# Kernel tuning notes

Hardware: AMD Instinct MI355X
Metric: run time of the kernel (lower is better)

The kernel has to match this reference:

```python
import jax, jax.numpy as jnp
import numpy as np

# UKF constants (Merwe scaled sigma points)
ALPHA, BETA, KAPPA = 1.0, 2.0, 0.0
JITTER = 1e-4
S_DIM, C_DIM, M_DIM, H_DIM = 8, 2, 4, 32


def setup_inputs() -> dict:
    B, T = 1024, 256
    key = jax.random.key(0)
    ks = jax.random.split(key, 11)
    inp = {
        "X0": 0.1 * jax.random.normal(ks[0], (B, S_DIM), dtype=jnp.float32),
        "u": jax.random.normal(ks[1], (B, T, C_DIM), dtype=jnp.float32),
        "y": jax.random.normal(ks[2], (B, T, M_DIM), dtype=jnp.float32),
        # learned process model f(x,u) = x + tanh([x;u] W1 + b1) W2 + b2
        "W1": 0.1 * jax.random.normal(ks[3], (S_DIM + C_DIM, H_DIM), dtype=jnp.float32),
        "b1": jnp.zeros((H_DIM,), dtype=jnp.float32),
        "W2": 0.1 * jax.random.normal(ks[4], (H_DIM, S_DIM), dtype=jnp.float32),
        "b2": jnp.zeros((S_DIM,), dtype=jnp.float32),
        # linear measurement model h(x) = Hm x
        "Hm": 0.3 * jax.random.normal(ks[5], (M_DIM, S_DIM), dtype=jnp.float32),
        # learned diagonal noise / initial covariance (softplus parameterized)
        "lq": -3.0 + 0.1 * jax.random.normal(ks[6], (S_DIM,), dtype=jnp.float32),
        "lr": -2.0 + 0.1 * jax.random.normal(ks[7], (M_DIM,), dtype=jnp.float32),
        "lp0": -1.0 + 0.1 * jax.random.normal(ks[8], (S_DIM,), dtype=jnp.float32),
    }
    return inp


def reference(X0, u, y, W1, b1, W2, b2, Hm, lq, lr, lp0):
    B, n = X0.shape
    T = u.shape[1]
    lam = ALPHA ** 2 * (n + KAPPA) - n
    c = n + lam
    Wm = jnp.concatenate([jnp.array([lam / c], dtype=X0.dtype),
                          jnp.full((2 * n,), 0.5 / c, dtype=X0.dtype)])
    Wc = Wm.at[0].add(1.0 - ALPHA ** 2 + BETA)
    I = jnp.eye(n, dtype=X0.dtype)

    Q = jnp.diag(jax.nn.softplus(lq))            # [n,n] process noise
    R = jnp.diag(jax.nn.softplus(lr))            # [m,m] measurement noise
    P0 = jnp.broadcast_to(jnp.diag(jax.nn.softplus(lp0)), (B, n, n))  # P0(X0)

    def f(pts, u_t):  # pts [B,2n+1,n], u_t [B,C]
        uu = jnp.broadcast_to(u_t[:, None, :], pts.shape[:2] + (u_t.shape[-1],))
        z = jnp.concatenate([pts, uu], axis=-1)
        return pts + jnp.tanh(z @ W1 + b1) @ W2 + b2

    def step(carry, inp_t):
        x, P = carry            # x [B,n], P [B,n,n]
        u_t, y_t = inp_t        # u at i-1, y at i
        # sigma points via Cholesky of scaled covariance
        L = jnp.linalg.cholesky(c * P + JITTER * I)
        offs = jnp.swapaxes(L, -1, -2)  # [B,n,n]: row i = i-th column of L
        pts = jnp.concatenate([x[:, None], x[:, None] + offs, x[:, None] - offs], axis=1)  # [B,2n+1,n]
        # predict
        pts_f = f(pts, u_t)
        x_pred = jnp.einsum('s,bsn->bn', Wm, pts_f)
        dx = pts_f - x_pred[:, None]
        P_pred = jnp.einsum('s,bsn,bsm->bnm', Wc, dx, dx) + Q
        P_pred = 0.5 * (P_pred + jnp.swapaxes(P_pred, -1, -2)) + JITTER * I
        # measurement update (linear h reused on propagated sigma points)
        y_pts = pts_f @ Hm.T
        y_pred = jnp.einsum('s,bsm->bm', Wm, y_pts)
        dy = y_pts - y_pred[:, None]
        Sy = jnp.einsum('s,bsi,bsj->bij', Wc, dy, dy) + R
        Sy = 0.5 * (Sy + jnp.swapaxes(Sy, -1, -2))
        Pxy = jnp.einsum('s,bsn,bsm->bnm', Wc, dx, dy)
        # K = Pxy Sy^{-1} via solve on Sy (SPD)
        K = jnp.swapaxes(jnp.linalg.solve(Sy, jnp.swapaxes(Pxy, -1, -2)), -1, -2)
        x_new = x_pred + jnp.einsum('bnm,bm->bn', K, y_t - y_pred)
        P_new = P_pred - K @ Sy @ jnp.swapaxes(K, -1, -2)
        P_new = 0.5 * (P_new + jnp.swapaxes(P_new, -1, -2)) + JITTER * I
        q_e = 0.5 * jnp.linalg.slogdet(P_pred)[1]  # [B]
        r_e = 0.5 * jnp.linalg.slogdet(Sy)[1]      # [B]
        return (x_new, P_new), (x_new, P_new, q_e, r_e)

    # steps i = 1..T-1 use u[:, i-1] and y[:, i]
    u_seq = jnp.swapaxes(u[:, :T - 1], 0, 1)  # [T-1,B,C]
    y_seq = jnp.swapaxes(y[:, 1:], 0, 1)      # [T-1,B,M]
    _, (Xs, Ps, qs, rs) = jax.lax.scan(step, (X0, P0), (u_seq, y_seq))

    X = jnp.concatenate([X0[:, None], jnp.swapaxes(Xs, 0, 1)], axis=1)        # [B,T,n]
    P = jnp.concatenate([P0[:, None], jnp.swapaxes(Ps, 0, 1)], axis=1)        # [B,T,n,n]
    zcol = jnp.zeros((X0.shape[0], 1), dtype=X0.dtype)
    q_entr = jnp.concatenate([zcol, jnp.swapaxes(qs, 0, 1)], axis=1)          # [B,T]
    r_entr = jnp.concatenate([zcol, jnp.swapaxes(rs, 0, 1)], axis=1)          # [B,T]
    return X, P, q_entr, r_entr
```

## Files before the change

kernel.cpp:

```cpp
#include <hip/hip_runtime.h>
#include <math.h>

#define B_LEN 1024
#define T_LEN 256
#define HST 36

__device__ __forceinline__ float fast_rcp(float x) { return __builtin_amdgcn_rcpf(x); }
__device__ __forceinline__ float fast_rsq(float x) { return __builtin_amdgcn_rsqf(x); }
__device__ __forceinline__ float fast_tanh(float x) {
    float e = __expf(2.0f * x);
    return 1.0f - 2.0f * fast_rcp(e + 1.0f);
}
__device__ __forceinline__ float softplus_f(float x) {
    return (x > 20.0f) ? x : log1pf(expf(x));
}

__global__ __launch_bounds__(128)
void ukf_kernel(const float* __restrict__ X0, const float* __restrict__ U,
                const float* __restrict__ Y,  const float* __restrict__ W1,
                const float* __restrict__ B1, const float* __restrict__ W2,
                const float* __restrict__ B2, const float* __restrict__ HM,
                const float* __restrict__ LQ, const float* __restrict__ LR,
                const float* __restrict__ LP0, float* __restrict__ out)
{
    const int tid  = threadIdx.x;
    const int wid  = tid >> 6;
    const int lane = tid & 63;
    const int b    = blockIdx.x;
    const int i8   = lane >> 3;
    const int j8   = lane & 7;
    const int h32  = lane & 31;
    const int p4   = tid >> 5;
    const int m4   = lane & 3;
    const int sy   = lane >> 2;
    const int s2   = tid >> 3;
    const int d2   = tid & 7;

    __shared__ float u_sh[T_LEN * 2];
    __shared__ float y_sh[T_LEN * 4];
    __shared__ __align__(16) float pts_sh[17 * 8];
    __shared__ __align__(16) float hid_sh[17 * HST];
    __shared__ __align__(16) float pf_sh[17 * 8];
    __shared__ __align__(16) float dx_sh[17 * 8];
    __shared__ __align__(16) float yp_sh[17 * 4];
    __shared__ float x_sh[8];
    __shared__ float xp_sh[8];
    __shared__ float ypred_sh[4];
    __shared__ float Sy_sh[16];
    __shared__ float L4_sh[16];
    __shared__ float Pxy_sh[32];
    __shared__ float K_sh[32];
    __shared__ float T1_sh[32];
    __shared__ float Pp_sh[64];

    for (int k = tid; k < T_LEN * 2; k += 128) u_sh[k] = U[(size_t)b * (T_LEN * 2) + k];
    for (int k = tid; k < T_LEN * 4; k += 128) y_sh[k] = Y[(size_t)b * (T_LEN * 4) + k];

    float w1r[10];
    #pragma unroll
    for (int d = 0; d < 10; ++d) w1r[d] = W1[d * 32 + h32];
    const float b1r = B1[h32];
    float w2r[32];
    #pragma unroll
    for (int h = 0; h < 32; ++h) w2r[h] = W2[h * 8 + d2];
    const float b2r = B2[d2];
    float hmr[8];
    #pragma unroll
    for (int d = 0; d < 8; ++d) hmr[d] = HM[m4 * 8 + d];

    const float qdiag = softplus_f(LQ[i8]);
    const float rdiag = softplus_f(LR[m4]);

    const size_t Xbase = (size_t)b * T_LEN * 8;
    const size_t Pbase = (size_t)B_LEN * T_LEN * 8  + (size_t)b * T_LEN * 64;
    const size_t qbase = (size_t)B_LEN * T_LEN * 72 + (size_t)b * T_LEN;
    const size_t rbase = (size_t)B_LEN * T_LEN * 73 + (size_t)b * T_LEN;

    float P = (i8 == j8) ? softplus_f(LP0[i8]) : 0.0f;
    if (tid < 8) x_sh[tid] = X0[b * 8 + tid];
    if (wid == 0) {
        if (lane < 8) out[Xbase + lane] = X0[b * 8 + lane];
        out[Pbase + lane] = P;
        if (lane == 0) { out[qbase] = 0.0f; out[rbase] = 0.0f; }
    }
    __syncthreads();

    for (int t = 1; t < T_LEN; ++t) {
        if (wid == 0) {
            float a = 8.0f * P + ((i8 == j8) ? 1e-4f : 0.0f);
            #pragma unroll
            for (int j = 0; j < 8; ++j) {
                float dj = __shfl(a, j * 9);
                float rv = fast_rsq(dj);
                if (j8 == j) a = (i8 == j) ? dj * rv : a * rv;
                float ci = __shfl(a, i8 * 8 + j);
                float cj = __shfl(a, j8 * 8 + j);
                if (i8 > j && j8 > j) a -= ci * cj;
            }
            const float Lx = (j8 <= i8) ? a : 0.0f;
            const float xi = x_sh[i8];
            if (j8 == 0) pts_sh[i8] = xi;
            pts_sh[(1 + j8) * 8 + i8] = xi + Lx;
            pts_sh[(9 + j8) * 8 + i8] = xi - Lx;
        }
        __syncthreads();

        {
            const float u0 = u_sh[(t - 1) * 2 + 0];
            const float u1 = u_sh[(t - 1) * 2 + 1];
            const float ub = b1r + u0 * w1r[8] + u1 * w1r[9];
            #pragma unroll
            for (int k = 0; k < 5; ++k) {
                int s = 4 * k + p4;
                if (s < 17) {
                    const float4 pa = *(const float4*)&pts_sh[s * 8];
                    const float4 pb = *(const float4*)&pts_sh[s * 8 + 4];
                    float acc = ub
                        + pa.x * w1r[0] + pa.y * w1r[1] + pa.z * w1r[2] + pa.w * w1r[3]
                        + pb.x * w1r[4] + pb.y * w1r[5] + pb.z * w1r[6] + pb.w * w1r[7];
                    hid_sh[s * HST + h32] = fast_tanh(acc);
                }
            }
        }
        __syncthreads();

        {
            float acc = b2r;
            #pragma unroll
            for (int h = 0; h < 32; h += 4) {
                const float4 hv = *(const float4*)&hid_sh[s2 * HST + h];
                acc += hv.x * w2r[h] + hv.y * w2r[h + 1] + hv.z * w2r[h + 2] + hv.w * w2r[h + 3];
            }
            pf_sh[s2 * 8 + d2] = pts_sh[s2 * 8 + d2] + acc;
            if (tid < 8) {
                float a16 = b2r;
                #pragma unroll
                for (int h = 0; h < 32; h += 4) {
                    const float4 hv = *(const float4*)&hid_sh[16 * HST + h];
                    a16 += hv.x * w2r[h] + hv.y * w2r[h + 1] + hv.z * w2r[h + 2] + hv.w * w2r[h + 3];
                }
                pf_sh[16 * 8 + tid] = pts_sh[16 * 8 + tid] + a16;
            }
        }
        __syncthreads();

        if (wid == 0) {
            const float v0   = pf_sh[i8 * 8 + j8];
            const float v1   = pf_sh[(8 + i8) * 8 + j8];
            const float pf16 = (i8 == 0) ? pf_sh[16 * 8 + j8] : 0.0f;
            float part = ((i8 == 0) ? pf16 : v0) + v1;
            part += __shfl_xor(part, 8);
            part += __shfl_xor(part, 16);
            part += __shfl_xor(part, 32);
            const float xp = part * 0.0625f;
            if (i8 == 0) xp_sh[j8] = xp;
            dx_sh[i8 * 8 + j8]       = v0 - xp;
            dx_sh[(8 + i8) * 8 + j8] = v1 - xp;
            if (i8 == 0) dx_sh[16 * 8 + j8] = pf16 - xp;
        } else {
            float yv0, yv16 = 0.0f;
            {
                const float4 pa = *(const float4*)&pf_sh[sy * 8];
                const float4 pb = *(const float4*)&pf_sh[sy * 8 + 4];
                yv0 = pa.x * hmr[0] + pa.y * hmr[1] + pa.z * hmr[2] + pa.w * hmr[3]
                    + pb.x * hmr[4] + pb.y * hmr[5] + pb.z * hmr[6] + pb.w * hmr[7];
            }
            if (sy == 0) {
                const float4 pa = *(const float4*)&pf_sh[16 * 8];
                const float4 pb = *(const float4*)&pf_sh[16 * 8 + 4];
                yv16 = pa.x * hmr[0] + pa.y * hmr[1] + pa.z * hmr[2] + pa.w * hmr[3]
                     + pb.x * hmr[4] + pb.y * hmr[5] + pb.z * hmr[6] + pb.w * hmr[7];
            }
            float py = (sy == 0) ? yv16 : yv0;
            py += __shfl_xor(py, 4);
            py += __shfl_xor(py, 8);
            py += __shfl_xor(py, 16);
            py += __shfl_xor(py, 32);
            const float ypred = py * 0.0625f;
            if (lane < 4) ypred_sh[lane] = ypred;
            yp_sh[sy * 4 + m4] = yv0 - ypred;
            if (sy == 0) yp_sh[16 * 4 + m4] = yv16 - ypred;
        }
        __syncthreads();

        float Ppred = 0.0f;
        if (wid == 0) {
            float pp = 0.0f;
            #pragma unroll
            for (int s = 1; s < 17; ++s)
                pp += dx_sh[s * 8 + i8] * dx_sh[s * 8 + j8];
            pp *= 0.0625f;
            pp += 2.0f * dx_sh[i8] * dx_sh[j8];
            Ppred = pp + ((i8 == j8) ? (qdiag + 1e-4f) : 0.0f);
            Pp_sh[lane] = Ppred;
        } else {
            if (lane < 16) {
                float acc = 0.0f;
                #pragma unroll
                for (int s = 1; s < 17; ++s)
                    acc += yp_sh[s * 4 + sy] * yp_sh[s * 4 + m4];
                Sy_sh[lane] = acc * 0.0625f + 2.0f * yp_sh[sy] * yp_sh[m4]
                            + ((sy == m4) ? rdiag : 0.0f);
            } else if (lane < 48) {
                const int idx = lane - 16;
                const int ii = idx >> 2, mm = idx & 3;
                float acc = 0.0f;
                #pragma unroll
                for (int s = 1; s < 17; ++s)
                    acc += dx_sh[s * 8 + ii] * yp_sh[s * 4 + mm];
                Pxy_sh[idx] = acc * 0.0625f + 2.0f * dx_sh[ii] * yp_sh[mm];
            }
        }
        __syncthreads();

        if (wid == 0) {
            float l4v = (lane < 16) ? Sy_sh[lane] : 0.0f;
            float re = 0.0f;
            #pragma unroll
            for (int j = 0; j < 4; ++j) {
                float dj = __shfl(l4v, j * 5);
                float rv = fast_rsq(dj);
                re += 0.5f * __logf(dj);
                if (lane < 16 && m4 == j) l4v = (sy == j) ? dj * rv : l4v * rv;
                float ci = __shfl(l4v, (sy * 4 + j) & 63);
                float cj = __shfl(l4v, (m4 * 4 + j) & 63);
                if (lane < 16 && sy > j && m4 > j) l4v -= ci * cj;
            }
            if (lane < 16) L4_sh[lane] = l4v;

            if (lane < 8) {
                const float p0  = Pxy_sh[lane * 4 + 0];
                const float p1  = Pxy_sh[lane * 4 + 1];
                const float p2v = Pxy_sh[lane * 4 + 2];
                const float p3  = Pxy_sh[lane * 4 + 3];
                const float L00 = L4_sh[0],  L10 = L4_sh[4],  L11 = L4_sh[5];
                const float L20 = L4_sh[8],  L21 = L4_sh[9],  L22 = L4_sh[10];
                const float L30 = L4_sh[12], L31 = L4_sh[13], L32 = L4_sh[14], L33 = L4_sh[15];
                const float r0 = fast_rcp(L00), r1 = fast_rcp(L11);
                const float r2 = fast_rcp(L22), r3 = fast_rcp(L33);
                const float w0_ = p0 * r0;
                const float w1_ = (p1 - L10 * w0_) * r1;
                const float w2_ = (p2v - L20 * w0_ - L21 * w1_) * r2;
                const float w3_ = (p3 - L30 * w0_ - L31 * w1_ - L32 * w2_) * r3;
                const float k3 = w3_ * r3;
                const float k2 = (w2_ - L32 * k3) * r2;
                const float k1 = (w1_ - L21 * k2 - L31 * k3) * r1;
                const float k0 = (w0_ - L10 * k1 - L20 * k2 - L30 * k3) * r0;
                K_sh[lane * 4 + 0] = k0;
                K_sh[lane * 4 + 1] = k1;
                K_sh[lane * 4 + 2] = k2;
                K_sh[lane * 4 + 3] = k3;
            }
            if (lane < 32) {
                const int ii = lane >> 2, aa = lane & 3;
                T1_sh[lane] = K_sh[ii * 4 + 0] * Sy_sh[0 + aa]
                            + K_sh[ii * 4 + 1] * Sy_sh[4 + aa]
                            + K_sh[ii * 4 + 2] * Sy_sh[8 + aa]
                            + K_sh[ii * 4 + 3] * Sy_sh[12 + aa];
            }
            float m_ = Ppred - (T1_sh[i8 * 4 + 0] * K_sh[j8 * 4 + 0]
                              + T1_sh[i8 * 4 + 1] * K_sh[j8 * 4 + 1]
                              + T1_sh[i8 * 4 + 2] * K_sh[j8 * 4 + 2]
                              + T1_sh[i8 * 4 + 3] * K_sh[j8 * 4 + 3]);
            float mT = __shfl(m_, j8 * 8 + i8);
            P = 0.5f * (m_ + mT) + ((i8 == j8) ? 1e-4f : 0.0f);
            out[Pbase + (size_t)t * 64 + lane] = P;

            if (lane < 8) {
                const float in0 = y_sh[t * 4 + 0] - ypred_sh[0];
                const float in1 = y_sh[t * 4 + 1] - ypred_sh[1];
                const float in2 = y_sh[t * 4 + 2] - ypred_sh[2];
                const float in3 = y_sh[t * 4 + 3] - ypred_sh[3];
                const float xn = xp_sh[lane]
                    + K_sh[lane * 4 + 0] * in0 + K_sh[lane * 4 + 1] * in1
                    + K_sh[lane * 4 + 2] * in2 + K_sh[lane * 4 + 3] * in3;
                x_sh[lane] = xn;
                out[Xbase + (size_t)t * 8 + lane] = xn;
            }
            if (lane == 0) out[rbase + t] = re;
        } else {
            float ap = Pp_sh[lane];
            float qe = 0.0f;
            #pragma unroll
            for (int j = 0; j < 8; ++j) {
                float dj = __shfl(ap, j * 9);
                float rv = fast_rsq(dj);
                qe += 0.5f * __logf(dj);
                if (j8 == j) ap = (i8 == j) ? dj * rv : ap * rv;
                float ci = __shfl(ap, i8 * 8 + j);
                float cj = __shfl(ap, j8 * 8 + j);
                if (i8 > j && j8 > j) ap -= ci * cj;
            }
            if (lane == 0) out[qbase + t] = qe;
        }
    }
}

extern "C" void kernel_launch(void* const* d_in, const int* in_sizes, int n_in,
                              void* d_out, int out_size, void* d_ws, size_t ws_size,
                              hipStream_t stream) {
    (void)in_sizes; (void)n_in; (void)out_size; (void)d_ws; (void)ws_size;
    const float* X0 = (const float*)d_in[0];
    const float* U  = (const float*)d_in[1];
    const float* Y  = (const float*)d_in[2];
    const float* W1 = (const float*)d_in[3];
    const float* B1 = (const float*)d_in[4];
    const float* W2 = (const float*)d_in[5];
    const float* B2 = (const float*)d_in[6];
    const float* HM = (const float*)d_in[7];
    const float* LQ = (const float*)d_in[8];
    const float* LR = (const float*)d_in[9];
    const float* LP0 = (const float*)d_in[10];
    float* out = (float*)d_out;
    ukf_kernel<<<dim3(B_LEN), dim3(128), 0, stream>>>(X0, U, Y, W1, B1, W2, B2,
                                                      HM, LQ, LR, LP0, out);
}
```

Baseline: 982.1 us.

## Keep covariance columns in registers and use readlane-based Cholesky

Covariance and state now live per-lane as column registers (each lane holds a column across eight rows). The 8x8 and 4x4 Cholesky factorizations use scalar readlane broadcasts instead of shuffles, and the 4x4 factor is computed redundantly in registers instead of going through shared memory. The MLP hidden and output stages are fused into one phase, removing a barrier, and launch bounds now request two blocks per CU. The goal is to cut shuffle and LDS traffic and barriers on the sequential per-timestep critical path, at the cost of more registers and redundant arithmetic across lanes.

```diff
diff --git a/kernel.cpp b/kernel.cpp
--- a/kernel.cpp
+++ b/kernel.cpp
@@ -7,6 +7,9 @@
 
 __device__ __forceinline__ float fast_rcp(float x) { return __builtin_amdgcn_rcpf(x); }
 __device__ __forceinline__ float fast_rsq(float x) { return __builtin_amdgcn_rsqf(x); }
+__device__ __forceinline__ float lane_bcast(float v, int l) {
+    return __int_as_float(__builtin_amdgcn_readlane(__float_as_int(v), l));
+}
 __device__ __forceinline__ float fast_tanh(float x) {
     float e = __expf(2.0f * x);
     return 1.0f - 2.0f * fast_rcp(e + 1.0f);
@@ -15,7 +18,7 @@
     return (x > 20.0f) ? x : log1pf(expf(x));
 }
 
-__global__ __launch_bounds__(128)
+__global__ __launch_bounds__(128, 2)
 void ukf_kernel(const float* __restrict__ X0, const float* __restrict__ U,
                 const float* __restrict__ Y,  const float* __restrict__ W1,
                 const float* __restrict__ B1, const float* __restrict__ W2,
@@ -27,31 +30,28 @@
     const int wid  = tid >> 6;
     const int lane = tid & 63;
     const int b    = blockIdx.x;
-    const int i8   = lane >> 3;
-    const int j8   = lane & 7;
+    const int k8   = lane & 7;
+    const int g8   = lane >> 3;
+    const int i8   = g8;
+    const int j8   = k8;
     const int h32  = lane & 31;
-    const int p4   = tid >> 5;
+    const int p2   = lane >> 5;
     const int m4   = lane & 3;
     const int sy   = lane >> 2;
-    const int s2   = tid >> 3;
-    const int d2   = tid & 7;
-
-    __shared__ float u_sh[T_LEN * 2];
-    __shared__ float y_sh[T_LEN * 4];
+
+    __shared__ __align__(16) float u_sh[T_LEN * 2];
+    __shared__ __align__(16) float y_sh[T_LEN * 4];
     __shared__ __align__(16) float pts_sh[17 * 8];
     __shared__ __align__(16) float hid_sh[17 * HST];
     __shared__ __align__(16) float pf_sh[17 * 8];
     __shared__ __align__(16) float dx_sh[17 * 8];
     __shared__ __align__(16) float yp_sh[17 * 4];
-    __shared__ float x_sh[8];
-    __shared__ float xp_sh[8];
-    __shared__ float ypred_sh[4];
-    __shared__ float Sy_sh[16];
-    __shared__ float L4_sh[16];
-    __shared__ float Pxy_sh[32];
-    __shared__ float K_sh[32];
-    __shared__ float T1_sh[32];
-    __shared__ float Pp_sh[64];
+    __shared__ __align__(16) float xp_sh[8];
+    __shared__ __align__(16) float ypred_sh[4];
+    __shared__ __align__(16) float Sy_sh[16];
+    __shared__ __align__(16) float Pxy_sh[32];
+    __shared__ __align__(16) float K_sh[32];
+    __shared__ __align__(16) float Pp_sh[64];
 
     for (int k = tid; k < T_LEN * 2; k += 128) u_sh[k] = U[(size_t)b * (T_LEN * 2) + k];
     for (int k = tid; k < T_LEN * 4; k += 128) y_sh[k] = Y[(size_t)b * (T_LEN * 4) + k];
@@ -62,8 +62,8 @@
     const float b1r = B1[h32];
     float w2r[32];
     #pragma unroll
-    for (int h = 0; h < 32; ++h) w2r[h] = W2[h * 8 + d2];
-    const float b2r = B2[d2];
+    for (int h = 0; h < 32; ++h) w2r[h] = W2[h * 8 + k8];
+    const float b2r = B2[k8];
     float hmr[8];
     #pragma unroll
     for (int d = 0; d < 8; ++d) hmr[d] = HM[m4 * 8 + d];
@@ -76,32 +76,68 @@
     const size_t qbase = (size_t)B_LEN * T_LEN * 72 + (size_t)b * T_LEN;
     const size_t rbase = (size_t)B_LEN * T_LEN * 73 + (size_t)b * T_LEN;
 
-    float P = (i8 == j8) ? softplus_f(LP0[i8]) : 0.0f;
-    if (tid < 8) x_sh[tid] = X0[b * 8 + tid];
+    float xn[8], Pc[8];
+    {
+        const float4 xa = *(const float4*)&X0[b * 8];
+        const float4 xb = *(const float4*)&X0[b * 8 + 4];
+        xn[0] = xa.x; xn[1] = xa.y; xn[2] = xa.z; xn[3] = xa.w;
+        xn[4] = xb.x; xn[5] = xb.y; xn[6] = xb.z; xn[7] = xb.w;
+        const float p0k = softplus_f(LP0[k8]);
+        #pragma unroll
+        for (int i = 0; i < 8; ++i) Pc[i] = (i == k8) ? p0k : 0.0f;
+    }
     if (wid == 0) {
-        if (lane < 8) out[Xbase + lane] = X0[b * 8 + lane];
-        out[Pbase + lane] = P;
-        if (lane == 0) { out[qbase] = 0.0f; out[rbase] = 0.0f; }
+        if (g8 == 0) {
+            #pragma unroll
+            for (int i = 0; i < 8; ++i) out[Pbase + i * 8 + k8] = Pc[i];
+        }
+        if (lane == 0) {
+            *(float4*)&out[Xbase]     = make_float4(xn[0], xn[1], xn[2], xn[3]);
+            *(float4*)&out[Xbase + 4] = make_float4(xn[4], xn[5], xn[6], xn[7]);
+            out[qbase] = 0.0f; out[rbase] = 0.0f;
+        }
     }
-    __syncthreads();
 
     for (int t = 1; t < T_LEN; ++t) {
         if (wid == 0) {
-            float a = 8.0f * P + ((i8 == j8) ? 1e-4f : 0.0f);
+            float a[8];
+            #pragma unroll
+            for (int i = 0; i < 8; ++i) a[i] = 8.0f * Pc[i] + ((i == k8) ? 1e-4f : 0.0f);
             #pragma unroll
             for (int j = 0; j < 8; ++j) {
-                float dj = __shfl(a, j * 9);
-                float rv = fast_rsq(dj);
-                if (j8 == j) a = (i8 == j) ? dj * rv : a * rv;
-                float ci = __shfl(a, i8 * 8 + j);
-                float cj = __shfl(a, j8 * 8 + j);
-                if (i8 > j && j8 > j) a -= ci * cj;
-            }
-            const float Lx = (j8 <= i8) ? a : 0.0f;
-            const float xi = x_sh[i8];
-            if (j8 == 0) pts_sh[i8] = xi;
-            pts_sh[(1 + j8) * 8 + i8] = xi + Lx;
-            pts_sh[(9 + j8) * 8 + i8] = xi - Lx;
+                const float dj  = lane_bcast(a[j], j);
+                const float rv  = fast_rsq(dj);
+                const float rv2 = rv * rv;
+                float u[8];
+                #pragma unroll
+                for (int i = j + 1; i < 8; ++i) u[i] = lane_bcast(a[i], j);
+                if (k8 == j) {
+                    a[j] = dj * rv;
+                    #pragma unroll
+                    for (int i = j + 1; i < 8; ++i) a[i] *= rv;
+                } else if (k8 > j) {
+                    const float tt = a[j] * rv2;
+                    #pragma unroll
+                    for (int i = j + 1; i < 8; ++i) a[i] = fmaf(-tt, u[i], a[i]);
+                }
+            }
+            float Lc[8];
+            #pragma unroll
+            for (int i = 0; i < 8; ++i) Lc[i] = (i >= k8) ? a[i] : 0.0f;
+            if (g8 == 0) {
+                *(float4*)&pts_sh[(1 + k8) * 8] =
+                    make_float4(xn[0] + Lc[0], xn[1] + Lc[1], xn[2] + Lc[2], xn[3] + Lc[3]);
+                *(float4*)&pts_sh[(1 + k8) * 8 + 4] =
+                    make_float4(xn[4] + Lc[4], xn[5] + Lc[5], xn[6] + Lc[6], xn[7] + Lc[7]);
+            } else if (g8 == 1) {
+                *(float4*)&pts_sh[(9 + k8) * 8] =
+                    make_float4(xn[0] - Lc[0], xn[1] - Lc[1], xn[2] - Lc[2], xn[3] - Lc[3]);
+                *(float4*)&pts_sh[(9 + k8) * 8 + 4] =
+                    make_float4(xn[4] - Lc[4], xn[5] - Lc[5], xn[6] - Lc[6], xn[7] - Lc[7]);
+            } else if (g8 == 2 && k8 == 0) {
+                *(float4*)&pts_sh[0] = make_float4(xn[0], xn[1], xn[2], xn[3]);
+                *(float4*)&pts_sh[4] = make_float4(xn[4], xn[5], xn[6], xn[7]);
+            }
         }
         __syncthreads();
 
@@ -109,10 +145,10 @@
             const float u0 = u_sh[(t - 1) * 2 + 0];
             const float u1 = u_sh[(t - 1) * 2 + 1];
             const float ub = b1r + u0 * w1r[8] + u1 * w1r[9];
-            #pragma unroll
-            for (int k = 0; k < 5; ++k) {
-                int s = 4 * k + p4;
-                if (s < 17) {
+            if (wid == 0) {
+                #pragma unroll
+                for (int p = 0; p < 4; ++p) {
+                    const int s = 2 * p + p2;
                     const float4 pa = *(const float4*)&pts_sh[s * 8];
                     const float4 pb = *(const float4*)&pts_sh[s * 8 + 4];
                     float acc = ub
@@ -120,26 +156,42 @@
                         + pb.x * w1r[4] + pb.y * w1r[5] + pb.z * w1r[6] + pb.w * w1r[7];
                     hid_sh[s * HST + h32] = fast_tanh(acc);
                 }
-            }
-        }
-        __syncthreads();
-
-        {
+            } else {
+                #pragma unroll
+                for (int p = 0; p < 4; ++p) {
+                    const int s = 8 + 2 * p + p2;
+                    const float4 pa = *(const float4*)&pts_sh[s * 8];
+                    const float4 pb = *(const float4*)&pts_sh[s * 8 + 4];
+                    float acc = ub
+                        + pa.x * w1r[0] + pa.y * w1r[1] + pa.z * w1r[2] + pa.w * w1r[3]
+                        + pb.x * w1r[4] + pb.y * w1r[5] + pb.z * w1r[6] + pb.w * w1r[7];
+                    hid_sh[s * HST + h32] = fast_tanh(acc);
+                }
+                if (p2 == 0) {
+                    const float4 pa = *(const float4*)&pts_sh[16 * 8];
+                    const float4 pb = *(const float4*)&pts_sh[16 * 8 + 4];
+                    float acc = ub
+                        + pa.x * w1r[0] + pa.y * w1r[1] + pa.z * w1r[2] + pa.w * w1r[3]
+                        + pb.x * w1r[4] + pb.y * w1r[5] + pb.z * w1r[6] + pb.w * w1r[7];
+                    hid_sh[16 * HST + h32] = fast_tanh(acc);
+                }
+            }
+            const int srow = (wid == 0) ? g8 : (8 + g8);
             float acc = b2r;
             #pragma unroll
             for (int h = 0; h < 32; h += 4) {
-                const float4 hv = *(const float4*)&hid_sh[s2 * HST + h];
+                const float4 hv = *(const float4*)&hid_sh[srow * HST + h];
                 acc += hv.x * w2r[h] + hv.y * w2r[h + 1] + hv.z * w2r[h + 2] + hv.w * w2r[h + 3];
             }
-            pf_sh[s2 * 8 + d2] = pts_sh[s2 * 8 + d2] + acc;
-            if (tid < 8) {
+            pf_sh[srow * 8 + k8] = pts_sh[srow * 8 + k8] + acc;
+            if (wid == 1 && lane < 8) {
                 float a16 = b2r;
                 #pragma unroll
                 for (int h = 0; h < 32; h += 4) {
                     const float4 hv = *(const float4*)&hid_sh[16 * HST + h];
                     a16 += hv.x * w2r[h] + hv.y * w2r[h + 1] + hv.z * w2r[h + 2] + hv.w * w2r[h + 3];
                 }
-                pf_sh[16 * 8 + tid] = pts_sh[16 * 8 + tid] + a16;
+                pf_sh[16 * 8 + lane] = pts_sh[16 * 8 + lane] + a16;
             }
         }
         __syncthreads();
@@ -183,7 +235,7 @@
         }
         __syncthreads();
 
-        float Ppred = 0.0f;
+        float Ppc[8];
         if (wid == 0) {
             float pp = 0.0f;
             #pragma unroll
@@ -191,8 +243,10 @@
                 pp += dx_sh[s * 8 + i8] * dx_sh[s * 8 + j8];
             pp *= 0.0625f;
             pp += 2.0f * dx_sh[i8] * dx_sh[j8];
-            Ppred = pp + ((i8 == j8) ? (qdiag + 1e-4f) : 0.0f);
+            const float Ppred = pp + ((i8 == j8) ? (qdiag + 1e-4f) : 0.0f);
             Pp_sh[lane] = Ppred;
+            #pragma unroll
+            for (int i = 0; i < 8; ++i) Ppc[i] = Pp_sh[i * 8 + k8];
         } else {
             if (lane < 16) {
                 float acc = 0.0f;
@@ -214,82 +268,99 @@
         __syncthreads();
 
         if (wid == 0) {
-            float l4v = (lane < 16) ? Sy_sh[lane] : 0.0f;
-            float re = 0.0f;
-            #pragma unroll
-            for (int j = 0; j < 4; ++j) {
-                float dj = __shfl(l4v, j * 5);
-                float rv = fast_rsq(dj);
-                re += 0.5f * __logf(dj);
-                if (lane < 16 && m4 == j) l4v = (sy == j) ? dj * rv : l4v * rv;
-                float ci = __shfl(l4v, (sy * 4 + j) & 63);
-                float cj = __shfl(l4v, (m4 * 4 + j) & 63);
-                if (lane < 16 && sy > j && m4 > j) l4v -= ci * cj;
-            }
-            if (lane < 16) L4_sh[lane] = l4v;
-
-            if (lane < 8) {
-                const float p0  = Pxy_sh[lane * 4 + 0];
-                const float p1  = Pxy_sh[lane * 4 + 1];
-                const float p2v = Pxy_sh[lane * 4 + 2];
-                const float p3  = Pxy_sh[lane * 4 + 3];
-                const float L00 = L4_sh[0],  L10 = L4_sh[4],  L11 = L4_sh[5];
-                const float L20 = L4_sh[8],  L21 = L4_sh[9],  L22 = L4_sh[10];
-                const float L30 = L4_sh[12], L31 = L4_sh[13], L32 = L4_sh[14], L33 = L4_sh[15];
-                const float r0 = fast_rcp(L00), r1 = fast_rcp(L11);
-                const float r2 = fast_rcp(L22), r3 = fast_rcp(L33);
-                const float w0_ = p0 * r0;
-                const float w1_ = (p1 - L10 * w0_) * r1;
-                const float w2_ = (p2v - L20 * w0_ - L21 * w1_) * r2;
-                const float w3_ = (p3 - L30 * w0_ - L31 * w1_ - L32 * w2_) * r3;
-                const float k3 = w3_ * r3;
-                const float k2 = (w2_ - L32 * k3) * r2;
-                const float k1 = (w1_ - L21 * k2 - L31 * k3) * r1;
-                const float k0 = (w0_ - L10 * k1 - L20 * k2 - L30 * k3) * r0;
-                K_sh[lane * 4 + 0] = k0;
-                K_sh[lane * 4 + 1] = k1;
-                K_sh[lane * 4 + 2] = k2;
-                K_sh[lane * 4 + 3] = k3;
-            }
-            if (lane < 32) {
-                const int ii = lane >> 2, aa = lane & 3;
-                T1_sh[lane] = K_sh[ii * 4 + 0] * Sy_sh[0 + aa]
-                            + K_sh[ii * 4 + 1] * Sy_sh[4 + aa]
-                            + K_sh[ii * 4 + 2] * Sy_sh[8 + aa]
-                            + K_sh[ii * 4 + 3] * Sy_sh[12 + aa];
-            }
-            float m_ = Ppred - (T1_sh[i8 * 4 + 0] * K_sh[j8 * 4 + 0]
-                              + T1_sh[i8 * 4 + 1] * K_sh[j8 * 4 + 1]
-                              + T1_sh[i8 * 4 + 2] * K_sh[j8 * 4 + 2]
-                              + T1_sh[i8 * 4 + 3] * K_sh[j8 * 4 + 3]);
-            float mT = __shfl(m_, j8 * 8 + i8);
-            P = 0.5f * (m_ + mT) + ((i8 == j8) ? 1e-4f : 0.0f);
-            out[Pbase + (size_t)t * 64 + lane] = P;
-
-            if (lane < 8) {
-                const float in0 = y_sh[t * 4 + 0] - ypred_sh[0];
-                const float in1 = y_sh[t * 4 + 1] - ypred_sh[1];
-                const float in2 = y_sh[t * 4 + 2] - ypred_sh[2];
-                const float in3 = y_sh[t * 4 + 3] - ypred_sh[3];
-                const float xn = xp_sh[lane]
-                    + K_sh[lane * 4 + 0] * in0 + K_sh[lane * 4 + 1] * in1
-                    + K_sh[lane * 4 + 2] * in2 + K_sh[lane * 4 + 3] * in3;
-                x_sh[lane] = xn;
-                out[Xbase + (size_t)t * 8 + lane] = xn;
-            }
-            if (lane == 0) out[rbase + t] = re;
+            float s_[16];
+            {
+                const float4 r0v = *(const float4*)&Sy_sh[0];
+                const float4 r1v = *(const float4*)&Sy_sh[4];
+                const float4 r2v = *(const float4*)&Sy_sh[8];
+                const float4 r3v = *(const float4*)&Sy_sh[12];
+                s_[0]=r0v.x;  s_[1]=r0v.y;  s_[2]=r0v.z;  s_[3]=r0v.w;
+                s_[4]=r1v.x;  s_[5]=r1v.y;  s_[6]=r1v.z;  s_[7]=r1v.w;
+                s_[8]=r2v.x;  s_[9]=r2v.y;  s_[10]=r2v.z; s_[11]=r2v.w;
+                s_[12]=r3v.x; s_[13]=r3v.y; s_[14]=r3v.z; s_[15]=r3v.w;
+            }
+            const float d0 = s_[0];
+            const float r0 = fast_rsq(d0);
+            const float L10 = s_[4] * r0, L20 = s_[8] * r0, L30 = s_[12] * r0;
+            const float d1 = s_[5] - L10 * L10;
+            const float r1 = fast_rsq(d1);
+            const float L21 = (s_[9]  - L20 * L10) * r1;
+            const float L31 = (s_[13] - L30 * L10) * r1;
+            const float d2_ = s_[10] - L20 * L20 - L21 * L21;
+            const float r2 = fast_rsq(d2_);
+            const float L32 = (s_[14] - L30 * L20 - L31 * L21) * r2;
+            const float d3 = s_[15] - L30 * L30 - L31 * L31 - L32 * L32;
+            const float r3 = fast_rsq(d3);
+            const float re = 0.5f * (__logf(d0) + __logf(d1) + __logf(d2_) + __logf(d3));
+
+            const float4 pr = *(const float4*)&Pxy_sh[k8 * 4];
+            const float w0_ = pr.x * r0;
+            const float w1_ = (pr.y - L10 * w0_) * r1;
+            const float w2_ = (pr.z - L20 * w0_ - L21 * w1_) * r2;
+            const float w3_ = (pr.w - L30 * w0_ - L31 * w1_ - L32 * w2_) * r3;
+            const float kk3 = w3_ * r3;
+            const float kk2 = (w2_ - L32 * kk3) * r2;
+            const float kk1 = (w1_ - L21 * kk2 - L31 * kk3) * r1;
+            const float kk0 = (w0_ - L10 * kk1 - L20 * kk2 - L30 * kk3) * r0;
+            if (g8 == 0) *(float4*)&K_sh[k8 * 4] = make_float4(kk0, kk1, kk2, kk3);
+
+            float K_[32];
+            #pragma unroll
+            for (int r = 0; r < 8; ++r) {
+                const float4 kr = *(const float4*)&K_sh[r * 4];
+                K_[r * 4 + 0] = kr.x; K_[r * 4 + 1] = kr.y;
+                K_[r * 4 + 2] = kr.z; K_[r * 4 + 3] = kr.w;
+            }
+            float w4[4];
+            #pragma unroll
+            for (int aa = 0; aa < 4; ++aa)
+                w4[aa] = s_[aa * 4 + 0] * kk0 + s_[aa * 4 + 1] * kk1
+                       + s_[aa * 4 + 2] * kk2 + s_[aa * 4 + 3] * kk3;
+            #pragma unroll
+            for (int i = 0; i < 8; ++i) {
+                const float m = K_[i * 4 + 0] * w4[0] + K_[i * 4 + 1] * w4[1]
+                              + K_[i * 4 + 2] * w4[2] + K_[i * 4 + 3] * w4[3];
+                Pc[i] = Ppc[i] - m + ((i == k8) ? 1e-4f : 0.0f);
+            }
+            const float4 yt = *(const float4*)&y_sh[t * 4];
+            const float4 yp = *(const float4*)&ypred_sh[0];
+            const float in0 = yt.x - yp.x, in1 = yt.y - yp.y;
+            const float in2 = yt.z - yp.z, in3 = yt.w - yp.w;
+            const float4 xpa = *(const float4*)&xp_sh[0];
+            const float4 xpb = *(const float4*)&xp_sh[4];
+            float xpv[8] = {xpa.x, xpa.y, xpa.z, xpa.w, xpb.x, xpb.y, xpb.z, xpb.w};
+            #pragma unroll
+            for (int i = 0; i < 8; ++i)
+                xn[i] = xpv[i] + K_[i * 4 + 0] * in0 + K_[i * 4 + 1] * in1
+                               + K_[i * 4 + 2] * in2 + K_[i * 4 + 3] * in3;
+            if (g8 == 0) {
+                #pragma unroll
+                for (int i = 0; i < 8; ++i)
+                    out[Pbase + (size_t)t * 64 + i * 8 + k8] = Pc[i];
+            }
+            if (lane == 0) {
+                *(float4*)&out[Xbase + (size_t)t * 8]     = make_float4(xn[0], xn[1], xn[2], xn[3]);
+                *(float4*)&out[Xbase + (size_t)t * 8 + 4] = make_float4(xn[4], xn[5], xn[6], xn[7]);
+                out[rbase + t] = re;
+            }
         } else {
-            float ap = Pp_sh[lane];
+            float aq[8];
+            #pragma unroll
+            for (int i = 0; i < 8; ++i) aq[i] = Pp_sh[i * 8 + k8];
             float qe = 0.0f;
             #pragma unroll
             for (int j = 0; j < 8; ++j) {
-                float dj = __shfl(ap, j * 9);
-                float rv = fast_rsq(dj);
+                const float dj  = lane_bcast(aq[j], j);
                 qe += 0.5f * __logf(dj);
-                if (j8 == j) ap = (i8 == j) ? dj * rv : ap * rv;
-                float ci = __shfl(ap, i8 * 8 + j);
-                float cj = __shfl(ap, j8 * 8 + j);
-                if (i8 > j && j8 > j) ap -= ci * cj;
+                const float rv2 = fast_rcp(dj);
+                float u[8];
+                #pragma unroll
+                for (int i = j + 1; i < 8; ++i) u[i] = lane_bcast(aq[i], j);
+                if (k8 > j) {
+                    const float tt = aq[j] * rv2;
+                    #pragma unroll
+                    for (int i = j + 1; i < 8; ++i) aq[i] = fmaf(-tt, u[i], aq[i]);
+                }
             }
             if (lane == 0) out[qbase + t] = qe;
         }
```

Result: no change. 965.6 us (-1.7%).
